# Kernel optimization log

Hardware: AMD Instinct MI355X
Metric: run time of the kernel (lower is better)

The kernel has to match this reference:

```python
import jax, jax.numpy as jnp
import numpy as np

N = 50000       # num nodes
E = 800000      # num edges (avg degree 16)
D = 128         # in_dim = hidden_dim = out_dim
C = 10          # n_classes
NOISE_STD = 0.1
LN_EPS = 1e-5


def layer_norm(x, g, b):
    mu = jnp.mean(x, axis=-1, keepdims=True)
    var = jnp.mean((x - mu) ** 2, axis=-1, keepdims=True)
    return (x - mu) * jax.lax.rsqrt(var + LN_EPS) * g + b


def gcn_conv(x, W, b, src, dst, dout_isqrt, din_isqrt):
    # DGL GraphConv, norm='both': h = D_in^{-1/2} A (D_out^{-1/2} x W) + b
    h = (x * dout_isqrt[:, None]) @ W              # [N, D] transform first (in>=out)
    agg = jax.ops.segment_sum(h[src], dst, num_segments=x.shape[0])  # SpMM via gather+scatter
    return agg * din_isqrt[:, None] + b


def setup_inputs() -> dict:
    key = jax.random.key(0)
    ks = jax.random.split(key, 16)
    inv = 1.0 / np.sqrt(D)
    return {
        "feat": jax.random.normal(ks[0], (N, D), jnp.float32),
        "noise": jax.random.normal(ks[1], (N, D), jnp.float32),
        "node_mask": jax.random.bernoulli(ks[2], 0.1, (N,)),
        "src": jax.random.randint(ks[3], (E,), 0, N, jnp.int32),
        "dst": jax.random.randint(ks[4], (E,), 0, N, jnp.int32),
        "mask_token": jax.random.normal(ks[5], (D,), jnp.float32) * inv,
        "W0": jax.random.normal(ks[6], (D, D), jnp.float32) * inv,
        "b0": jnp.zeros((D,), jnp.float32),
        "ln0_g": jnp.ones((D,), jnp.float32),
        "ln0_b": jnp.zeros((D,), jnp.float32),
        "W1": jax.random.normal(ks[7], (D, D), jnp.float32) * inv,
        "b1": jnp.zeros((D,), jnp.float32),
        "ln1_g": jnp.ones((D,), jnp.float32),
        "ln1_b": jnp.zeros((D,), jnp.float32),
        "dec_W1": jax.random.normal(ks[8], (D, D), jnp.float32) * inv,
        "dec_b1": jnp.zeros((D,), jnp.float32),
        "dec_W2": jax.random.normal(ks[9], (D, D), jnp.float32) * inv,
        "dec_b2": jnp.zeros((D,), jnp.float32),
        "cls_W": jax.random.normal(ks[10], (D, C), jnp.float32) * inv,
        "cls_b": jnp.zeros((C,), jnp.float32),
    }


def reference(feat, noise, node_mask, src, dst, mask_token,
              W0, b0, ln0_g, ln0_b, W1, b1, ln1_g, ln1_b,
              dec_W1, dec_b1, dec_W2, dec_b2, cls_W, cls_b):
    n = feat.shape[0]
    ones_e = jnp.ones(src.shape, feat.dtype)
    deg_out = jax.ops.segment_sum(ones_e, src, num_segments=n)
    deg_in = jax.ops.segment_sum(ones_e, dst, num_segments=n)
    dout_isqrt = jnp.where(deg_out > 0, jax.lax.rsqrt(jnp.maximum(deg_out, 1.0)), 0.0)
    din_isqrt = jnp.where(deg_in > 0, jax.lax.rsqrt(jnp.maximum(deg_in, 1.0)), 0.0)

    # node masking + noise injection (eval mode: dropout is identity)
    x_masked = jnp.where(node_mask[:, None], mask_token[None, :], feat) + noise * NOISE_STD

    # encoder: layer 0 (conv -> LN -> ReLU), layer 1 (conv -> LN)
    h = gcn_conv(x_masked, W0, b0, src, dst, dout_isqrt, din_isqrt)
    h = jax.nn.relu(layer_norm(h, ln0_g, ln0_b))
    h = gcn_conv(h, W1, b1, src, dst, dout_isqrt, din_isqrt)
    z = layer_norm(h, ln1_g, ln1_b)

    x_recon = jax.nn.relu(z @ dec_W1 + dec_b1) @ dec_W2 + dec_b2
    logits = z @ cls_W + cls_b
    return (x_recon, feat, node_mask, z, logits)
```

## Files before the change

kernel.cpp:

```cpp
#include <hip/hip_runtime.h>
#include <hip/hip_bf16.h>

#define LN_EPS 1e-5f
#define HB 64
#define HSEG 12800
#define NBLK 128
#define BROWS 64
#define WPSTRIDE 17408

typedef __attribute__((ext_vector_type(8))) short short8;
typedef __attribute__((ext_vector_type(4))) float f32x4;

__device__ __forceinline__ unsigned short f2bf(float f) {
    unsigned int u = __float_as_uint(f);
    u += 0x7fffu + ((u >> 16) & 1u);
    return (unsigned short)(u >> 16);
}
__device__ __forceinline__ unsigned int pack2bf(float a, float b) {
    return (unsigned int)f2bf(a) | ((unsigned int)f2bf(b) << 16);
}
__device__ __forceinline__ float bflo(unsigned int v) { return __uint_as_float(v << 16); }
__device__ __forceinline__ float bfhi(unsigned int v) { return __uint_as_float(v & 0xffff0000u); }

__global__ __launch_bounds__(256) void k_front(const int* __restrict__ src, int* __restrict__ partials,
                                               const int* __restrict__ dst, int* __restrict__ counts,
                                               const float* __restrict__ Wa, const float* __restrict__ Wb,
                                               const float* __restrict__ Wc, const float* __restrict__ Wd,
                                               unsigned short* __restrict__ wpack,
                                               const float* __restrict__ feat, const float* __restrict__ noise,
                                               const int* __restrict__ mask, const float* __restrict__ token,
                                               unsigned short* __restrict__ xs, float* __restrict__ feat_out,
                                               float* __restrict__ mask_out,
                                               int nbuck, int E, int n, int N) {
    __shared__ int h[HSEG];
    int bid = blockIdx.x;
    int tid = threadIdx.x;
    if (bid < 256) {
        int chunk = bid & (HB - 1);
        int seg = bid >> 6;
        int lo = seg * HSEG;
        int len = N - lo;
        if (len > HSEG) len = HSEG;
        if (len <= 0) return;
        for (int i = tid; i < len; i += 256) h[i] = 0;
        __syncthreads();
        int per = (E + HB - 1) / HB;
        int e0 = chunk * per, e1 = min(e0 + per, E);
        for (int e = e0 + tid; e < e1; e += 256) {
            int s = src[e] - lo;
            if ((unsigned)s < (unsigned)len) atomicAdd(&h[s], 1);
        }
        __syncthreads();
        for (int i = tid; i < len; i += 256)
            partials[(size_t)chunk * N + lo + i] = h[i];
        return;
    }
    bid -= 256;
    if (bid < NBLK) {
        for (int i = tid; i < nbuck; i += 256) h[i] = 0;
        __syncthreads();
        int per = (E + NBLK - 1) / NBLK;
        int e0 = bid * per, e1 = min(e0 + per, E);
        for (int e = e0 + tid; e < e1; e += 256) atomicAdd(&h[dst[e] >> 6], 1);
        __syncthreads();
        for (int i = tid; i < nbuck; i += 256) counts[(size_t)i * NBLK + bid] = h[i];
        return;
    }
    bid -= NBLK;
    if (bid < 256) {
        int idx = bid * 256 + tid;
        int wsel = idx >> 14;
        int within = idx & 16383;
        const float* W = wsel == 0 ? Wa : wsel == 1 ? Wb : wsel == 2 ? Wc : Wd;
        int c = within >> 7, kk = within & 127;
        wpack[(size_t)wsel * WPSTRIDE + c * 136 + kk] = f2bf(W[kk * 128 + c]);
        return;
    }
    bid -= 256;
    int i = bid * 256 + tid;
    int total = n * 32;
    if (i >= total) return;
    int row = i >> 5, q = i & 31;
    float4 f = ((const float4*)feat)[i];
    float4 nz = ((const float4*)noise)[i];
    bool m = mask[row] != 0;
    float4 b = f;
    if (m) b = ((const float4*)token)[q];
    uint2 p;
    p.x = pack2bf(b.x + 0.1f * nz.x, b.y + 0.1f * nz.y);
    p.y = pack2bf(b.z + 0.1f * nz.z, b.w + 0.1f * nz.w);
    ((uint2*)xs)[i] = p;
    ((float4*)feat_out)[i] = f;
    if (q == 0) mask_out[row] = m ? 1.0f : 0.0f;
}

__global__ __launch_bounds__(128) void k_mid1(const int* __restrict__ counts, int* __restrict__ tot,
                                              const int* __restrict__ partials, float* __restrict__ doutv,
                                              int nbuck, int N) {
    int t = threadIdx.x;
    int bid = blockIdx.x;
    if (bid < nbuck) {
        __shared__ int sm[128];
        sm[t] = counts[(size_t)bid * NBLK + t];
        __syncthreads();
#pragma unroll
        for (int o = 64; o >= 1; o >>= 1) {
            if (t < o) sm[t] += sm[t + o];
            __syncthreads();
        }
        if (t == 0) tot[bid] = sm[0];
        return;
    }
    int i = (bid - nbuck) * 128 + t;
    if (i >= N) return;
    int s = 0;
#pragma unroll
    for (int b = 0; b < HB; ++b) s += partials[(size_t)b * N + i];
    doutv[i] = s > 0 ? 1.0f / sqrtf((float)s) : 0.0f;
}

__global__ __launch_bounds__(128) void k_binB3(const int* __restrict__ counts, const int* __restrict__ tot,
                                               int* __restrict__ base, int* __restrict__ offs,
                                               int nbuck, int E) {
    __shared__ int sm[128];
    __shared__ int pref[128];
    int b = blockIdx.x, t = threadIdx.x;
    int ps = 0;
    for (int j = t; j < b; j += 128) ps += tot[j];
    pref[t] = ps;
    __syncthreads();
#pragma unroll
    for (int o = 64; o >= 1; o >>= 1) {
        if (t < o) pref[t] += pref[t + o];
        __syncthreads();
    }
    int gbase = pref[0];
    int v = counts[(size_t)b * NBLK + t];
    sm[t] = v;
    __syncthreads();
    for (int o = 1; o < 128; o <<= 1) {
        int u = (t >= o) ? sm[t - o] : 0;
        __syncthreads();
        sm[t] += u;
        __syncthreads();
    }
    offs[(size_t)b * NBLK + t] = gbase + sm[t] - v;
    if (t == 127) {
        base[b] = gbase;
        if (b == nbuck - 1) base[nbuck] = E;
    }
}

__global__ __launch_bounds__(256) void k_binC(const int* __restrict__ src, const int* __restrict__ dst,
                                              const int* __restrict__ offs, uint2* __restrict__ binned,
                                              int nbuck, int E) {
    __shared__ int cur[1024];
    for (int i = threadIdx.x; i < nbuck; i += 256) cur[i] = offs[(size_t)i * NBLK + blockIdx.x];
    __syncthreads();
    int per = (E + NBLK - 1) / NBLK;
    int e0 = blockIdx.x * per, e1 = min(e0 + per, E);
    for (int e = e0 + threadIdx.x; e < e1; e += 256) {
        int d = dst[e];
        int p = atomicAdd(&cur[d >> 6], 1);
        binned[p] = make_uint2((unsigned)src[e], (unsigned)d);
    }
}

__global__ __launch_bounds__(256) void k_csr(const uint2* __restrict__ binned, const int* __restrict__ base,
                                             int* __restrict__ row_ptr, int* __restrict__ csr_src, int N) {
    __shared__ int hcnt[BROWS], ccur[BROWS];
    int b = blockIdx.x, t = threadIdx.x;
    int e0 = base[b], e1 = base[b + 1];
    if (t < BROWS) hcnt[t] = 0;
    __syncthreads();
    for (int e = e0 + t; e < e1; e += 256)
        atomicAdd(&hcnt[binned[e].y & (BROWS - 1)], 1);
    __syncthreads();
    if (t < BROWS) {
        int acc = 0;
        for (int r = 0; r < t; ++r) acc += hcnt[r];
        ccur[t] = acc;
        int gw = b * BROWS + t;
        if (gw <= N) row_ptr[gw] = e0 + acc;
    }
    __syncthreads();
    for (int e = e0 + t; e < e1; e += 256) {
        uint2 ed = binned[e];
        int p = atomicAdd(&ccur[ed.y & (BROWS - 1)], 1);
        csr_src[e0 + p] = (int)ed.x;
    }
}

template <int EPI, int OUT_BF16, int DOUT>
__global__ __launch_bounds__(256) void k_gemm_mfma(const unsigned short* __restrict__ A,
                                                   const unsigned short* __restrict__ Wp,
                                                   const float* __restrict__ bias,
                                                   const float* __restrict__ dscale,
                                                   void* __restrict__ Cout, int n) {
    __shared__ uint4 BtV[2176];
    unsigned short* Bt = (unsigned short*)BtV;
    int tid = threadIdx.x;
    const uint4* Wv = (const uint4*)Wp;
    for (int i = tid; i < 2176; i += 256) BtV[i] = Wv[i];
    __syncthreads();

    int wid = tid >> 6, lane = tid & 63;
    int q = lane >> 4, m = lane & 15;
    int r0 = blockIdx.x * 128 + wid * 32;

    f32x4 acc[2][8];
#pragma unroll
    for (int i = 0; i < 2; ++i)
#pragma unroll
        for (int j = 0; j < 8; ++j) acc[i][j] = (f32x4){0.f, 0.f, 0.f, 0.f};

#pragma unroll
    for (int ks = 0; ks < 4; ++ks) {
        int k0 = ks * 32 + q * 8;
        short8 a[2];
#pragma unroll
        for (int i = 0; i < 2; ++i) {
            int row = r0 + i * 16 + m;
            if (row > n - 1) row = n - 1;
            a[i] = *(const short8*)(A + (size_t)row * 128 + k0);
        }
        short8 b[8];
#pragma unroll
        for (int j = 0; j < 8; ++j)
            b[j] = *(const short8*)(&Bt[(j * 16 + m) * 136 + k0]);
#pragma unroll
        for (int i = 0; i < 2; ++i)
#pragma unroll
            for (int j = 0; j < 8; ++j)
                acc[i][j] = __builtin_amdgcn_mfma_f32_16x16x32_bf16(a[i], b[j], acc[i][j], 0, 0, 0);
    }

    float bv[8];
    if (EPI >= 1) {
#pragma unroll
        for (int j = 0; j < 8; ++j) bv[j] = bias[j * 16 + m];
    }

#pragma unroll
    for (int i = 0; i < 2; ++i) {
#pragma unroll
        for (int r = 0; r < 4; ++r) {
            int row = r0 + i * 16 + q * 4 + r;
            if (row < n) {
                float ds = DOUT ? dscale[row] : 1.0f;
#pragma unroll
                for (int j = 0; j < 8; ++j) {
                    float v = acc[i][j][r];
                    if (DOUT) v *= ds;
                    if (EPI >= 1) v += bv[j];
                    if (EPI == 2) v = fmaxf(v, 0.0f);
                    if (OUT_BF16)
                        ((unsigned short*)Cout)[(size_t)row * 128 + j * 16 + m] = f2bf(v);
                    else
                        ((float*)Cout)[(size_t)row * 128 + j * 16 + m] = v;
                }
            }
        }
    }
}

__global__ __launch_bounds__(256) void k_dec(const unsigned short* __restrict__ A,
                                             const unsigned short* __restrict__ Wp1, const float* __restrict__ bias1,
                                             const unsigned short* __restrict__ Wp2, const float* __restrict__ bias2,
                                             float* __restrict__ Cout,
                                             const float* __restrict__ cW, const float* __restrict__ cbias,
                                             float* __restrict__ logits,
                                             int n, int C, int gb) {
    __shared__ uint4 W1V[2176];
    __shared__ uint4 W2V[2176];
    int tid = threadIdx.x;
    if ((int)blockIdx.x >= gb) {
        int gpos = ((int)blockIdx.x - gb) * 256 + tid;
        int row = gpos >> 4, c = gpos & 15;
        if (row >= n || c >= C) return;
        const unsigned int* zr = (const unsigned int*)(A + (size_t)row * 128);
        float acc = cbias[c];
#pragma unroll 8
        for (int kk = 0; kk < 64; ++kk) {
            unsigned int v = zr[kk];
            acc = fmaf(bflo(v), cW[(2 * kk) * C + c], acc);
            acc = fmaf(bfhi(v), cW[(2 * kk + 1) * C + c], acc);
        }
        logits[(size_t)row * C + c] = acc;
        return;
    }
    const uint4* w1 = (const uint4*)Wp1;
    const uint4* w2 = (const uint4*)Wp2;
    for (int i = tid; i < 2176; i += 256) { W1V[i] = w1[i]; W2V[i] = w2[i]; }
    __syncthreads();
    unsigned short* W1s = (unsigned short*)W1V;
    unsigned short* W2s = (unsigned short*)W2V;

    int wid = tid >> 6, lane = tid & 63;
    int q = lane >> 4, m = lane & 15;
    int r0 = blockIdx.x * 128 + wid * 32;

    f32x4 acc[2][8];
#pragma unroll
    for (int i = 0; i < 2; ++i)
#pragma unroll
        for (int j = 0; j < 8; ++j) acc[i][j] = (f32x4){0.f, 0.f, 0.f, 0.f};
#pragma unroll
    for (int ks = 0; ks < 4; ++ks) {
        int k0 = ks * 32 + q * 8;
        short8 a[2];
#pragma unroll
        for (int i = 0; i < 2; ++i) {
            int row = r0 + i * 16 + m;
            if (row > n - 1) row = n - 1;
            a[i] = *(const short8*)(A + (size_t)row * 128 + k0);
        }
        short8 b[8];
#pragma unroll
        for (int j = 0; j < 8; ++j)
            b[j] = *(const short8*)(&W1s[(j * 16 + m) * 136 + k0]);
#pragma unroll
        for (int i = 0; i < 2; ++i)
#pragma unroll
            for (int j = 0; j < 8; ++j)
                acc[i][j] = __builtin_amdgcn_mfma_f32_16x16x32_bf16(a[i], b[j], acc[i][j], 0, 0, 0);
    }
    float bv[8];
#pragma unroll
    for (int j = 0; j < 8; ++j) bv[j] = bias1[j * 16 + m];

    __syncthreads();
    unsigned short* T = W1s;
#pragma unroll
    for (int i = 0; i < 2; ++i)
#pragma unroll
        for (int r = 0; r < 4; ++r) {
            int lrow = wid * 32 + i * 16 + q * 4 + r;
#pragma unroll
            for (int j = 0; j < 8; ++j) {
                float v = acc[i][j][r] + bv[j];
                T[lrow * 136 + j * 16 + m] = f2bf(fmaxf(v, 0.0f));
            }
        }
    __syncthreads();

#pragma unroll
    for (int i = 0; i < 2; ++i)
#pragma unroll
        for (int j = 0; j < 8; ++j) acc[i][j] = (f32x4){0.f, 0.f, 0.f, 0.f};
#pragma unroll
    for (int ks = 0; ks < 4; ++ks) {
        int k0 = ks * 32 + q * 8;
        short8 a[2];
#pragma unroll
        for (int i = 0; i < 2; ++i)
            a[i] = *(const short8*)(&T[(wid * 32 + i * 16 + m) * 136 + k0]);
        short8 b[8];
#pragma unroll
        for (int j = 0; j < 8; ++j)
            b[j] = *(const short8*)(&W2s[(j * 16 + m) * 136 + k0]);
#pragma unroll
        for (int i = 0; i < 2; ++i)
#pragma unroll
            for (int j = 0; j < 8; ++j)
                acc[i][j] = __builtin_amdgcn_mfma_f32_16x16x32_bf16(a[i], b[j], acc[i][j], 0, 0, 0);
    }
#pragma unroll
    for (int j = 0; j < 8; ++j) bv[j] = bias2[j * 16 + m];
#pragma unroll
    for (int i = 0; i < 2; ++i)
#pragma unroll
        for (int r = 0; r < 4; ++r) {
            int row = r0 + i * 16 + q * 4 + r;
            if (row < n) {
#pragma unroll
                for (int j = 0; j < 8; ++j)
                    Cout[(size_t)row * 128 + j * 16 + m] = acc[i][j][r] + bv[j];
            }
        }
}

template <int MODE>
__global__ __launch_bounds__(256) void k_agg_ln(const unsigned short* __restrict__ H,
                                                const int* __restrict__ row_ptr,
                                                const int* __restrict__ csr_src,
                                                const float* __restrict__ cb, const float* __restrict__ g,
                                                const float* __restrict__ bt,
                                                float* __restrict__ out_f32, unsigned short* __restrict__ out_bf,
                                                int n) {
    int gw = (blockIdx.x * blockDim.x + threadIdx.x) >> 6;
    int lane = threadIdx.x & 63;
    if (gw >= n) return;
    int beg = row_ptr[gw], end = row_ptr[gw + 1];
    int cnt = end - beg;
    const uint2* H2 = (const uint2*)H;
    int half = lane >> 5;
    int hl = lane & 31;
    float a0 = 0.f, a1 = 0.f, a2 = 0.f, a3 = 0.f;
    for (int c0 = beg; c0 < end; c0 += 64) {
        int m = end - c0;
        if (m > 64) m = 64;
        int myidx = (lane < m) ? csr_src[c0 + lane] : 0;
        int k = 0;
        for (; k + 15 < m; k += 16) {
            uint2 v[8];
#pragma unroll
            for (int p = 0; p < 8; ++p) {
                int s = __shfl(myidx, k + 2 * p + half);
                v[p] = H2[(size_t)s * 32 + hl];
            }
#pragma unroll
            for (int p = 0; p < 8; ++p) {
                a0 += bflo(v[p].x); a1 += bfhi(v[p].x);
                a2 += bflo(v[p].y); a3 += bfhi(v[p].y);
            }
        }
        for (; k + 7 < m; k += 8) {
            uint2 v[4];
#pragma unroll
            for (int p = 0; p < 4; ++p) {
                int s = __shfl(myidx, k + 2 * p + half);
                v[p] = H2[(size_t)s * 32 + hl];
            }
#pragma unroll
            for (int p = 0; p < 4; ++p) {
                a0 += bflo(v[p].x); a1 += bfhi(v[p].x);
                a2 += bflo(v[p].y); a3 += bfhi(v[p].y);
            }
        }
        for (; k < m; k += 2) {
            int e = k + half;
            int s = __shfl(myidx, (e < m) ? e : k);
            uint2 vv = H2[(size_t)s * 32 + hl];
            if (e < m) {
                a0 += bflo(vv.x); a1 += bfhi(vv.x);
                a2 += bflo(vv.y); a3 += bfhi(vv.y);
            }
        }
    }
    a0 += __shfl_xor(a0, 32, 64);
    a1 += __shfl_xor(a1, 32, 64);
    a2 += __shfl_xor(a2, 32, 64);
    a3 += __shfl_xor(a3, 32, 64);

    int d0 = hl * 4;
    float sc = cnt > 0 ? 1.0f / sqrtf((float)cnt) : 0.0f;
    float4 cbv = *(const float4*)(cb + d0);
    float x0 = a0 * sc + cbv.x;
    float x1 = a1 * sc + cbv.y;
    float x2 = a2 * sc + cbv.z;
    float x3 = a3 * sc + cbv.w;

    float s = x0 + x1 + x2 + x3;
#pragma unroll
    for (int mm = 16; mm >= 1; mm >>= 1) s += __shfl_xor(s, mm, 64);
    float mu = s * (1.0f / 128.0f);
    float dx0 = x0 - mu, dx1 = x1 - mu, dx2 = x2 - mu, dx3 = x3 - mu;
    float v = dx0 * dx0 + dx1 * dx1 + dx2 * dx2 + dx3 * dx3;
#pragma unroll
    for (int mm = 16; mm >= 1; mm >>= 1) v += __shfl_xor(v, mm, 64);
    float inv = 1.0f / sqrtf(v * (1.0f / 128.0f) + LN_EPS);
    float4 gv = *(const float4*)(g + d0);
    float4 bvv = *(const float4*)(bt + d0);
    float y0 = dx0 * inv * gv.x + bvv.x;
    float y1 = dx1 * inv * gv.y + bvv.y;
    float y2 = dx2 * inv * gv.z + bvv.z;
    float y3 = dx3 * inv * gv.w + bvv.w;
    if (MODE == 1) {
        y0 = fmaxf(y0, 0.0f); y1 = fmaxf(y1, 0.0f);
        y2 = fmaxf(y2, 0.0f); y3 = fmaxf(y3, 0.0f);
    }
    if (half == 0) {
        if (MODE == 0) {
            float4 z4 = make_float4(y0, y1, y2, y3);
            *(float4*)(out_f32 + (size_t)gw * 128 + d0) = z4;
        }
        uint2 pk;
        pk.x = pack2bf(y0, y1);
        pk.y = pack2bf(y2, y3);
        ((uint2*)out_bf)[(size_t)gw * 32 + hl] = pk;
    }
}

extern "C" void kernel_launch(void* const* d_in, const int* in_sizes, int n_in,
                              void* d_out, int out_size, void* d_ws, size_t ws_size,
                              hipStream_t stream) {
    const float* feat  = (const float*)d_in[0];
    const float* noise = (const float*)d_in[1];
    const int*   nmask = (const int*)d_in[2];
    const int*   src   = (const int*)d_in[3];
    const int*   dst   = (const int*)d_in[4];
    const float* token = (const float*)d_in[5];
    const float* W0    = (const float*)d_in[6];
    const float* b0    = (const float*)d_in[7];
    const float* ln0g  = (const float*)d_in[8];
    const float* ln0b  = (const float*)d_in[9];
    const float* W1    = (const float*)d_in[10];
    const float* b1    = (const float*)d_in[11];
    const float* ln1g  = (const float*)d_in[12];
    const float* ln1b  = (const float*)d_in[13];
    const float* dW1   = (const float*)d_in[14];
    const float* db1   = (const float*)d_in[15];
    const float* dW2   = (const float*)d_in[16];
    const float* db2   = (const float*)d_in[17];
    const float* cW    = (const float*)d_in[18];
    const float* cbias = (const float*)d_in[19];

    const int N = in_sizes[0] / 128;
    const int E = in_sizes[3];
    const int C = in_sizes[19];
    const size_t ND = (size_t)N * 128;
    const int NBUCK = (N + BROWS - 1) / BROWS;

    float* out       = (float*)d_out;
    float* out_recon = out;
    float* out_feat  = out + ND;
    float* out_mask  = out + 2 * ND;
    float* out_z     = out + 2 * ND + N;
    float* out_log   = out + 3 * ND + N;

    char* w = (char*)d_ws;
    unsigned short* bufX = (unsigned short*)w; w += ND * 2;
    unsigned short* bufH = (unsigned short*)w; w += ND * 2;
    unsigned short* zbf  = (unsigned short*)w; w += ND * 2;
    unsigned short* wpack = (unsigned short*)w; w += (size_t)4 * WPSTRIDE * 2;
    float* doutv   = (float*)w; w += (size_t)N * 4;
    int* row_ptr   = (int*)w;   w += (size_t)(N + 4) * 4;
    int* csr_src   = (int*)w;   w += (size_t)E * 4;
    int* scratch   = (int*)w;

    int* partials = scratch;
    uint2* binned = (uint2*)scratch;
    int* counts = scratch + (size_t)HB * N;
    int* tot    = counts + (size_t)NBUCK * NBLK;
    int* base   = tot + NBUCK;
    int* offs   = base + NBUCK + 2;

    int prep_blocks = (N * 32 + 255) / 256;
    k_front<<<256 + NBLK + 256 + prep_blocks, 256, 0, stream>>>(
        src, partials, dst, counts, W0, W1, dW1, dW2, wpack,
        feat, noise, nmask, token, bufX, out_feat, out_mask, NBUCK, E, N, N);

    int nr = (N + 127) / 128;
    k_mid1<<<NBUCK + nr, 128, 0, stream>>>(counts, tot, partials, doutv, NBUCK, N);

    k_binB3<<<NBUCK, 128, 0, stream>>>(counts, tot, base, offs, NBUCK, E);

    k_binC<<<NBLK, 256, 0, stream>>>(src, dst, offs, binned, NBUCK, E);
    k_csr<<<NBUCK, 256, 0, stream>>>(binned, base, row_ptr, csr_src, N);

    int gb = (N + 127) / 128;
    int rb = (N * 64 + 255) / 256;

    k_gemm_mfma<0, 1, 1><<<gb, 256, 0, stream>>>(bufX, wpack + 0 * WPSTRIDE, nullptr, doutv, bufH, N);
    k_agg_ln<1><<<rb, 256, 0, stream>>>(bufH, row_ptr, csr_src, b0, ln0g, ln0b, nullptr, bufX, N);

    k_gemm_mfma<0, 1, 1><<<gb, 256, 0, stream>>>(bufX, wpack + 1 * WPSTRIDE, nullptr, doutv, bufH, N);
    k_agg_ln<0><<<rb, 256, 0, stream>>>(bufH, row_ptr, csr_src, b1, ln1g, ln1b, out_z, zbf, N);

    int cls_blocks = (N * 16 + 255) / 256;
    k_dec<<<gb + cls_blocks, 256, 0, stream>>>(zbf, wpack + 2 * WPSTRIDE, db1, wpack + 3 * WPSTRIDE, db2,
                                               out_recon, cW, cbias, out_log, N, C, gb);
}
```

Baseline: 188.7 us.

## Split GCN aggregation into feature-sliced gather plus separate LayerNorm apply

The GEMM now writes H in a sliced layout, four 32-column slices each stored contiguously over all nodes. A new aggregation kernel gathers one slice per block, and the block ordering interleaves slices so each gather pass works on a quarter-size table that fits better in cache. It writes unnormalized bf16 sums plus per-slice sum and sum-of-squares partials. A second kernel combines the partials, applies LayerNorm and writes the outputs. This trades an extra launch, an intermediate buffer round-trip and a one-pass variance formula for better cache locality during the random gathers.

```diff
diff --git a/kernel.cpp b/kernel.cpp
--- a/kernel.cpp
+++ b/kernel.cpp
@@ -191,7 +191,7 @@
     }
 }
 
-template <int EPI, int OUT_BF16, int DOUT>
+template <int EPI, int OUT, int DOUT>
 __global__ __launch_bounds__(256) void k_gemm_mfma(const unsigned short* __restrict__ A,
                                                    const unsigned short* __restrict__ Wp,
                                                    const float* __restrict__ bias,
@@ -254,14 +254,113 @@
                     if (DOUT) v *= ds;
                     if (EPI >= 1) v += bv[j];
                     if (EPI == 2) v = fmaxf(v, 0.0f);
-                    if (OUT_BF16)
+                    if (OUT == 2) {
+                        ((unsigned short*)Cout)[((size_t)(j >> 1) * n + row) * 32 + (j & 1) * 16 + m] = f2bf(v);
+                    } else if (OUT == 1) {
                         ((unsigned short*)Cout)[(size_t)row * 128 + j * 16 + m] = f2bf(v);
-                    else
+                    } else {
                         ((float*)Cout)[(size_t)row * 128 + j * 16 + m] = v;
+                    }
                 }
             }
         }
     }
+}
+
+__global__ __launch_bounds__(256) void k_agg_slice(const unsigned short* __restrict__ Hp,
+                                                   const int* __restrict__ row_ptr,
+                                                   const int* __restrict__ csr_src,
+                                                   const float* __restrict__ cb,
+                                                   unsigned short* __restrict__ xp,
+                                                   float* __restrict__ part, int n) {
+    int bid = blockIdx.x;
+    int s = (bid & 7) >> 1;
+    int idx = (bid >> 3) * 2 + (bid & 1);
+    int wid = threadIdx.x >> 6, lane = threadIdx.x & 63;
+    int row = idx * 4 + wid;
+    if (row >= n) return;
+    int beg = row_ptr[row], end = row_ptr[row + 1];
+    int cnt = end - beg;
+    const uint2* P = (const uint2*)(Hp + (size_t)s * n * 32);
+    int egrp = lane >> 3, dl = lane & 7;
+    float a0 = 0.f, a1 = 0.f, a2 = 0.f, a3 = 0.f;
+    for (int c0 = beg; c0 < end; c0 += 64) {
+        int m = end - c0;
+        if (m > 64) m = 64;
+        int myidx = (lane < m) ? __builtin_nontemporal_load(csr_src + c0 + lane) : 0;
+        for (int k = 0; k < m; k += 16) {
+            int e0 = k + egrp, e1 = k + 8 + egrp;
+            int s0 = __shfl(myidx, e0 < m ? e0 : 0, 64);
+            int s1 = __shfl(myidx, e1 < m ? e1 : 0, 64);
+            uint2 v0 = P[(size_t)s0 * 8 + dl];
+            uint2 v1 = P[(size_t)s1 * 8 + dl];
+            if (e0 < m) { a0 += bflo(v0.x); a1 += bfhi(v0.x); a2 += bflo(v0.y); a3 += bfhi(v0.y); }
+            if (e1 < m) { a0 += bflo(v1.x); a1 += bfhi(v1.x); a2 += bflo(v1.y); a3 += bfhi(v1.y); }
+        }
+    }
+#pragma unroll
+    for (int o = 8; o < 64; o <<= 1) {
+        a0 += __shfl_xor(a0, o, 64);
+        a1 += __shfl_xor(a1, o, 64);
+        a2 += __shfl_xor(a2, o, 64);
+        a3 += __shfl_xor(a3, o, 64);
+    }
+    float sc = cnt > 0 ? 1.0f / sqrtf((float)cnt) : 0.0f;
+    float4 cbv = *(const float4*)(cb + s * 32 + dl * 4);
+    float x0 = a0 * sc + cbv.x;
+    float x1 = a1 * sc + cbv.y;
+    float x2 = a2 * sc + cbv.z;
+    float x3 = a3 * sc + cbv.w;
+    float p = x0 + x1 + x2 + x3;
+    float qq = x0 * x0 + x1 * x1 + x2 * x2 + x3 * x3;
+#pragma unroll
+    for (int o = 1; o < 8; o <<= 1) {
+        p += __shfl_xor(p, o, 64);
+        qq += __shfl_xor(qq, o, 64);
+    }
+    if (egrp == 0) {
+        unsigned long long pk = (unsigned long long)pack2bf(x0, x1) |
+                                ((unsigned long long)pack2bf(x2, x3) << 32);
+        __builtin_nontemporal_store(pk, (unsigned long long*)xp + ((size_t)s * n + row) * 8 + dl);
+        if (dl == 0) {
+            float2 pq = make_float2(p, qq);
+            __builtin_nontemporal_store(*(const double*)&pq,
+                                        (double*)part + (size_t)row * 4 + s);
+        }
+    }
+}
+
+template <int MODE>
+__global__ __launch_bounds__(256) void k_ln_apply(const unsigned short* __restrict__ xp,
+                                                  const float* __restrict__ part,
+                                                  const float* __restrict__ g, const float* __restrict__ bt,
+                                                  float* __restrict__ out_f32,
+                                                  unsigned short* __restrict__ out_bf, int n) {
+    int row = (blockIdx.x * 256 + threadIdx.x) >> 6;
+    int lane = threadIdx.x & 63;
+    if (row >= n) return;
+    float4 pa = *(const float4*)(part + (size_t)row * 8);
+    float4 pb = *(const float4*)(part + (size_t)row * 8 + 4);
+    float sum = pa.x + pa.z + pb.x + pb.z;
+    float sq  = pa.y + pa.w + pb.y + pb.w;
+    float mu = sum * (1.0f / 128.0f);
+    float var = sq * (1.0f / 128.0f) - mu * mu;
+    float inv = 1.0f / sqrtf(var + LN_EPS);
+    int s = lane >> 4, w = lane & 15;
+    unsigned int v = ((const unsigned int*)xp)[((size_t)s * n + row) * 16 + w];
+    float x0 = bflo(v), x1 = bfhi(v);
+    int d0 = lane * 2;
+    float2 gv = *(const float2*)(g + d0);
+    float2 bv = *(const float2*)(bt + d0);
+    float y0 = (x0 - mu) * inv * gv.x + bv.x;
+    float y1 = (x1 - mu) * inv * gv.y + bv.y;
+    if (MODE == 1) {
+        y0 = fmaxf(y0, 0.0f);
+        y1 = fmaxf(y1, 0.0f);
+    } else {
+        *(float2*)(out_f32 + (size_t)row * 128 + d0) = make_float2(y0, y1);
+    }
+    ((unsigned int*)out_bf)[(size_t)row * 64 + lane] = pack2bf(y0, y1);
 }
 
 __global__ __launch_bounds__(256) void k_dec(const unsigned short* __restrict__ A,
@@ -378,108 +477,6 @@
                     Cout[(size_t)row * 128 + j * 16 + m] = acc[i][j][r] + bv[j];
             }
         }
-}
-
-template <int MODE>
-__global__ __launch_bounds__(256) void k_agg_ln(const unsigned short* __restrict__ H,
-                                                const int* __restrict__ row_ptr,
-                                                const int* __restrict__ csr_src,
-                                                const float* __restrict__ cb, const float* __restrict__ g,
-                                                const float* __restrict__ bt,
-                                                float* __restrict__ out_f32, unsigned short* __restrict__ out_bf,
-                                                int n) {
-    int gw = (blockIdx.x * blockDim.x + threadIdx.x) >> 6;
-    int lane = threadIdx.x & 63;
-    if (gw >= n) return;
-    int beg = row_ptr[gw], end = row_ptr[gw + 1];
-    int cnt = end - beg;
-    const uint2* H2 = (const uint2*)H;
-    int half = lane >> 5;
-    int hl = lane & 31;
-    float a0 = 0.f, a1 = 0.f, a2 = 0.f, a3 = 0.f;
-    for (int c0 = beg; c0 < end; c0 += 64) {
-        int m = end - c0;
-        if (m > 64) m = 64;
-        int myidx = (lane < m) ? csr_src[c0 + lane] : 0;
-        int k = 0;
-        for (; k + 15 < m; k += 16) {
-            uint2 v[8];
-#pragma unroll
-            for (int p = 0; p < 8; ++p) {
-                int s = __shfl(myidx, k + 2 * p + half);
-                v[p] = H2[(size_t)s * 32 + hl];
-            }
-#pragma unroll
-            for (int p = 0; p < 8; ++p) {
-                a0 += bflo(v[p].x); a1 += bfhi(v[p].x);
-                a2 += bflo(v[p].y); a3 += bfhi(v[p].y);
-            }
-        }
-        for (; k + 7 < m; k += 8) {
-            uint2 v[4];
-#pragma unroll
-            for (int p = 0; p < 4; ++p) {
-                int s = __shfl(myidx, k + 2 * p + half);
-                v[p] = H2[(size_t)s * 32 + hl];
-            }
-#pragma unroll
-            for (int p = 0; p < 4; ++p) {
-                a0 += bflo(v[p].x); a1 += bfhi(v[p].x);
-                a2 += bflo(v[p].y); a3 += bfhi(v[p].y);
-            }
-        }
-        for (; k < m; k += 2) {
-            int e = k + half;
-            int s = __shfl(myidx, (e < m) ? e : k);
-            uint2 vv = H2[(size_t)s * 32 + hl];
-            if (e < m) {
-                a0 += bflo(vv.x); a1 += bfhi(vv.x);
-                a2 += bflo(vv.y); a3 += bfhi(vv.y);
-            }
-        }
-    }
-    a0 += __shfl_xor(a0, 32, 64);
-    a1 += __shfl_xor(a1, 32, 64);
-    a2 += __shfl_xor(a2, 32, 64);
-    a3 += __shfl_xor(a3, 32, 64);
-
-    int d0 = hl * 4;
-    float sc = cnt > 0 ? 1.0f / sqrtf((float)cnt) : 0.0f;
-    float4 cbv = *(const float4*)(cb + d0);
-    float x0 = a0 * sc + cbv.x;
-    float x1 = a1 * sc + cbv.y;
-    float x2 = a2 * sc + cbv.z;
-    float x3 = a3 * sc + cbv.w;
-
-    float s = x0 + x1 + x2 + x3;
-#pragma unroll
-    for (int mm = 16; mm >= 1; mm >>= 1) s += __shfl_xor(s, mm, 64);
-    float mu = s * (1.0f / 128.0f);
-    float dx0 = x0 - mu, dx1 = x1 - mu, dx2 = x2 - mu, dx3 = x3 - mu;
-    float v = dx0 * dx0 + dx1 * dx1 + dx2 * dx2 + dx3 * dx3;
-#pragma unroll
-    for (int mm = 16; mm >= 1; mm >>= 1) v += __shfl_xor(v, mm, 64);
-    float inv = 1.0f / sqrtf(v * (1.0f / 128.0f) + LN_EPS);
-    float4 gv = *(const float4*)(g + d0);
-    float4 bvv = *(const float4*)(bt + d0);
-    float y0 = dx0 * inv * gv.x + bvv.x;
-    float y1 = dx1 * inv * gv.y + bvv.y;
-    float y2 = dx2 * inv * gv.z + bvv.z;
-    float y3 = dx3 * inv * gv.w + bvv.w;
-    if (MODE == 1) {
-        y0 = fmaxf(y0, 0.0f); y1 = fmaxf(y1, 0.0f);
-        y2 = fmaxf(y2, 0.0f); y3 = fmaxf(y3, 0.0f);
-    }
-    if (half == 0) {
-        if (MODE == 0) {
-            float4 z4 = make_float4(y0, y1, y2, y3);
-            *(float4*)(out_f32 + (size_t)gw * 128 + d0) = z4;
-        }
-        uint2 pk;
-        pk.x = pack2bf(y0, y1);
-        pk.y = pack2bf(y2, y3);
-        ((uint2*)out_bf)[(size_t)gw * 32 + hl] = pk;
-    }
 }
 
 extern "C" void kernel_launch(void* const* d_in, const int* in_sizes, int n_in,
@@ -522,9 +519,11 @@
     char* w = (char*)d_ws;
     unsigned short* bufX = (unsigned short*)w; w += ND * 2;
     unsigned short* bufH = (unsigned short*)w; w += ND * 2;
+    unsigned short* xq   = (unsigned short*)w; w += ND * 2;
     unsigned short* zbf  = (unsigned short*)w; w += ND * 2;
     unsigned short* wpack = (unsigned short*)w; w += (size_t)4 * WPSTRIDE * 2;
     float* doutv   = (float*)w; w += (size_t)N * 4;
+    float* part    = (float*)w; w += (size_t)N * 8 * 4;
     int* row_ptr   = (int*)w;   w += (size_t)(N + 4) * 4;
     int* csr_src   = (int*)w;   w += (size_t)E * 4;
     int* scratch   = (int*)w;
@@ -543,20 +542,21 @@
 
     int nr = (N + 127) / 128;
     k_mid1<<<NBUCK + nr, 128, 0, stream>>>(counts, tot, partials, doutv, NBUCK, N);
-
     k_binB3<<<NBUCK, 128, 0, stream>>>(counts, tot, base, offs, NBUCK, E);
-
     k_binC<<<NBLK, 256, 0, stream>>>(src, dst, offs, binned, NBUCK, E);
     k_csr<<<NBUCK, 256, 0, stream>>>(binned, base, row_ptr, csr_src, N);
 
     int gb = (N + 127) / 128;
     int rb = (N * 64 + 255) / 256;
-
-    k_gemm_mfma<0, 1, 1><<<gb, 256, 0, stream>>>(bufX, wpack + 0 * WPSTRIDE, nullptr, doutv, bufH, N);
-    k_agg_ln<1><<<rb, 256, 0, stream>>>(bufH, row_ptr, csr_src, b0, ln0g, ln0b, nullptr, bufX, N);
-
-    k_gemm_mfma<0, 1, 1><<<gb, 256, 0, stream>>>(bufX, wpack + 1 * WPSTRIDE, nullptr, doutv, bufH, N);
-    k_agg_ln<0><<<rb, 256, 0, stream>>>(bufH, row_ptr, csr_src, b1, ln1g, ln1b, out_z, zbf, N);
+    int ab = (((N + 3) / 4 + 1) / 2) * 8;
+
+    k_gemm_mfma<0, 2, 1><<<gb, 256, 0, stream>>>(bufX, wpack + 0 * WPSTRIDE, nullptr, doutv, bufH, N);
+    k_agg_slice<<<ab, 256, 0, stream>>>(bufH, row_ptr, csr_src, b0, xq, part, N);
+    k_ln_apply<1><<<rb, 256, 0, stream>>>(xq, part, ln0g, ln0b, nullptr, bufX, N);
+
+    k_gemm_mfma<0, 2, 1><<<gb, 256, 0, stream>>>(bufX, wpack + 1 * WPSTRIDE, nullptr, doutv, bufH, N);
+    k_agg_slice<<<ab, 256, 0, stream>>>(bufH, row_ptr, csr_src, b1, xq, part, N);
+    k_ln_apply<0><<<rb, 256, 0, stream>>>(xq, part, ln1g, ln1b, out_z, zbf, N);
 
     int cls_blocks = (N * 16 + 255) / 256;
     k_dec<<<gb + cls_blocks, 256, 0, stream>>>(zbf, wpack + 2 * WPSTRIDE, db1, wpack + 3 * WPSTRIDE, db2,
```

New measurement: 301.3 us. +59.7%, slower.
